# Performance work log

Hardware: AMD Instinct MI355X
Metric: run time of the kernel (lower is better)

The kernel has to match this reference:

```python
import jax, jax.numpy as jnp
import numpy as np

F_, H_, W_ = 8, 24, 24          # video_shape
KS, DIL = 3, 1                  # kernel_size, dilation (cubic)
HEADS, DH, DIM = 8, 64, 512
N_TOK = F_ * H_ * W_            # 4608 video tokens (+1 BOS)
PAD = DIL * (KS - 1) // 2
SCALE = DH ** -0.5


def _geometry():
    """Precompute im2col gather indices into the padded volume and the causal mask."""
    fp, hp, wp = F_ + 2 * PAD, H_ + 2 * PAD, W_ + 2 * PAD
    tg, ig, jg = np.meshgrid(np.arange(F_), np.arange(H_), np.arange(W_), indexing='ij')
    a = np.arange(KS) * DIL
    at, ai, aj = np.meshgrid(a, a, a, indexing='ij')  # window offsets
    # query (t,i,j) in original coords == window start in padded coords
    tc = tg.reshape(-1, 1) + at.reshape(1, -1)  # [N, K3]
    ic = ig.reshape(-1, 1) + ai.reshape(1, -1)
    jc = jg.reshape(-1, 1) + aj.reshape(1, -1)
    idx = (tc * hp + ic) * wp + jc              # flat index into padded volume
    # token-id volume padded with sentinel N_TOK (matches F.pad value=max_num_tokens)
    tok = np.full((fp, hp, wp), N_TOK, dtype=np.int64)
    tok[PAD:PAD + F_, PAD:PAD + H_, PAD:PAD + W_] = np.arange(N_TOK).reshape(F_, H_, W_)
    unfolded = tok.reshape(-1)[idx]             # [N, K3]
    causal = np.arange(N_TOK)[:, None] < unfolded  # True = masked (padding is N_TOK > all)
    mask = np.concatenate([np.zeros((N_TOK, 1), bool), causal], axis=1)  # BOS never masked
    return idx, mask

_IDX_NP, _MASK_NP = _geometry()


def setup_inputs() -> dict:
    key = jax.random.key(0)
    ks = jax.random.split(key, 6)
    n = N_TOK + 1
    return {
        'x': jax.random.normal(ks[0], (1, n, DIM), jnp.float32),
        'w_q': jax.random.normal(ks[1], (DIM, HEADS * DH), jnp.float32) * 0.02,
        'w_kv': jax.random.normal(ks[2], (DIM, 2 * HEADS * DH), jnp.float32) * 0.02,
        'w_talk': jax.random.normal(ks[3], (HEADS, HEADS), jnp.float32) * 0.1,
        'w_out': jax.random.normal(ks[4], (HEADS * DH, DIM), jnp.float32) * 0.02,
        'b_out': jnp.zeros((DIM,), jnp.float32),
    }


def reference(x, w_q, w_kv, w_talk, w_out, b_out):
    idx = jnp.asarray(_IDX_NP)
    mask = jnp.asarray(_MASK_NP)
    b, n, _ = x.shape
    bh = b * HEADS
    fp, hp, wp = F_ + 2 * PAD, H_ + 2 * PAD, W_ + 2 * PAD

    q = x @ w_q                                  # [b, n, h*d]
    k, v = jnp.split(x @ w_kv, 2, axis=-1)

    def to_heads(t):
        return t.reshape(b, n, HEADS, DH).transpose(0, 2, 1, 3).reshape(bh, n, DH)

    q, k, v = map(to_heads, (q, k, v))
    q = q[:, 1:] * SCALE                         # drop BOS query
    k_bos, v_bos = k[:, :1], v[:, :1]            # [bh, 1, d]
    k, v = k[:, 1:], v[:, 1:]

    def pad_unfold(t):
        vol = t.reshape(bh, F_, H_, W_, DH)
        vol = jnp.pad(vol, ((0, 0), (PAD, PAD), (PAD, PAD), (PAD, PAD), (0, 0)))
        flat = vol.reshape(bh, fp * hp * wp, DH)
        return flat[:, idx]                      # [bh, N, K3, d]

    k_unf, v_unf = pad_unfold(k), pad_unfold(v)
    k_full = jnp.concatenate([jnp.broadcast_to(k_bos[:, None], (bh, N_TOK, 1, DH)), k_unf], axis=2)
    v_full = jnp.concatenate([jnp.broadcast_to(v_bos[:, None], (bh, N_TOK, 1, DH)), v_unf], axis=2)

    sim = jnp.einsum('bid,bijd->bij', q, k_full)           # [bh, N, 1+K3]
    sim = jnp.where(mask[None], -jnp.finfo(sim.dtype).max, sim)
    attn = jax.nn.softmax(sim, axis=-1)
    attn = attn.reshape(b, HEADS, N_TOK, -1)
    attn = jnp.einsum('gh,bhij->bgij', w_talk, attn)       # talking heads (1x1 conv)
    attn = attn.reshape(bh, N_TOK, -1)

    out = jnp.einsum('bij,bijd->bid', attn, v_full)        # [bh, N, d]
    out = jnp.concatenate([v_bos, out], axis=1)            # BOS output = v_bos
    out = out.reshape(b, HEADS, n, DH).transpose(0, 2, 1, 3).reshape(b, n, HEADS * DH)
    return out @ w_out + b_out
```

## Files before the change

### kernel.cpp

```cpp
#include <hip/hip_runtime.h>
#include <cfloat>
#include <cmath>

#define F_   8
#define H_   24
#define W_   24
#define NTOK 4608
#define NSEQ 4609
#define MPAD 4736
#define DIM  512
#define QKVC 1536
#define NNB  28
#define SCALEF 0.125f

typedef unsigned short ushort_t;
typedef __attribute__((ext_vector_type(8))) short short8v;
typedef __attribute__((ext_vector_type(8))) unsigned short ushort8v;
typedef __attribute__((ext_vector_type(4))) float floatx4;

typedef const __attribute__((address_space(1))) unsigned int guint_t;
typedef __attribute__((address_space(3))) unsigned int luint_t;

__device__ __forceinline__ float bf2f(unsigned short u) {
    return __uint_as_float(((unsigned)u) << 16);
}
__device__ __forceinline__ unsigned short f2bf(float f) {
    unsigned u = __float_as_uint(f);
    unsigned r = (u + 0x7FFFu + ((u >> 16) & 1u)) >> 16;
    return (unsigned short)r;
}

#define XBLK 1184
#define CONV_BLOCKS (XBLK + 192 + 64)

__global__ __launch_bounds__(256) void conv_k(
    const float* __restrict__ x, const float* __restrict__ wq,
    const float* __restrict__ wkv, const float* __restrict__ wout,
    ushort_t* __restrict__ xb, ushort_t* __restrict__ wcatT,
    ushort_t* __restrict__ woutT)
{
    const int bid = blockIdx.x, tid = threadIdx.x;
    __shared__ ushort_t tile[64][72];

    if (bid < XBLK) {
        int e0 = (bid * 256 + tid) * 8;
        int row = e0 >> 9;
        float4 a = make_float4(0.f, 0.f, 0.f, 0.f);
        float4 b = make_float4(0.f, 0.f, 0.f, 0.f);
        if (row < NSEQ) {
            a = *reinterpret_cast<const float4*>(&x[e0]);
            b = *reinterpret_cast<const float4*>(&x[e0 + 4]);
        }
        ushort8v o;
        o[0] = f2bf(a.x); o[1] = f2bf(a.y); o[2] = f2bf(a.z); o[3] = f2bf(a.w);
        o[4] = f2bf(b.x); o[5] = f2bf(b.y); o[6] = f2bf(b.z); o[7] = f2bf(b.w);
        *reinterpret_cast<ushort8v*>(&xb[e0]) = o;
        return;
    }

    int blk2 = bid - XBLK;
    const float* src; int ld, cb; ushort_t* dst; int k0;
    if (blk2 < 192) {
        int nt = blk2 >> 3, kt = blk2 & 7;
        int n0 = nt * 64;
        if (n0 < 512) { src = wq;  ld = 512;  cb = n0; }
        else          { src = wkv; ld = 1024; cb = n0 - 512; }
        dst = wcatT + (size_t)n0 * 512;
        k0 = kt * 64;
    } else {
        int b3 = blk2 - 192;
        int nt = b3 >> 3, kt = b3 & 7;
        src = wout; ld = 512; cb = nt * 64;
        dst = woutT + (size_t)(nt * 64) * 512;
        k0 = kt * 64;
    }

    {
        int r = tid >> 4, c4 = (tid & 15) * 4;
        #pragma unroll
        for (int p = 0; p < 4; ++p) {
            int rr = r + p * 16;
            float4 v = *reinterpret_cast<const float4*>(&src[(size_t)(k0 + rr) * ld + cb + c4]);
            tile[c4 + 0][rr] = f2bf(v.x);
            tile[c4 + 1][rr] = f2bf(v.y);
            tile[c4 + 2][rr] = f2bf(v.z);
            tile[c4 + 3][rr] = f2bf(v.w);
        }
    }
    __syncthreads();
    {
        int nl = tid >> 3, ks = (tid & 7) * 8;
        #pragma unroll
        for (int rep = 0; rep < 2; ++rep) {
            int nn = nl + rep * 32;
            ushort8v vv = *reinterpret_cast<const ushort8v*>(&tile[nn][ks]);
            *reinterpret_cast<ushort8v*>(&dst[(size_t)nn * 512 + k0 + ks]) = vv;
        }
    }
}

template<int BM, bool F32OUT>
__global__ __launch_bounds__(256, 4) void gemm_k(
    const ushort_t* __restrict__ A,
    const ushort_t* __restrict__ BT,
    const float* __restrict__ bias,
    void* __restrict__ Cv, int ldc)
{
    __shared__ ushort_t sA[BM * 64];
    __shared__ ushort_t sB[128 * 64];
    const int tid = threadIdx.x;

    const int nwg = gridDim.x * gridDim.y;
    const int orig = blockIdx.y * gridDim.x + blockIdx.x;
    const int xcd = orig & 7;
    const int qq = nwg >> 3, rr8 = nwg & 7;
    const int wg = (xcd < rr8 ? xcd * (qq + 1) : rr8 * (qq + 1) + (xcd - rr8) * qq)
                   + (orig >> 3);
    const int row0 = (wg / gridDim.x) * BM;
    const int col0 = (wg % gridDim.x) * 128;

    const int wid = tid >> 6, lane = tid & 63;
    const int wr = wid >> 1, wc = wid & 1;
    const int l15 = lane & 15, kp = lane >> 4;
    constexpr int MR = BM / 32;

    floatx4 acc[MR][4];
    #pragma unroll
    for (int m = 0; m < MR; ++m)
        #pragma unroll
        for (int n = 0; n < 4; ++n)
            acc[m][n] = (floatx4){0.f, 0.f, 0.f, 0.f};

    const ushort_t* Abase = A + (size_t)row0 * 512;
    const ushort_t* Bbase = BT + (size_t)col0 * 512;

    for (int kt = 0; kt < 8; ++kt) {
        const int k0 = kt * 64;
        #pragma unroll
        for (int rnd = 0; rnd < BM / 32; ++rnd) {
            int r = rnd * 32 + (tid >> 3);
            int gs = (tid & 7) ^ (r & 7);
            __builtin_amdgcn_global_load_lds(
                (guint_t*)(Abase + (size_t)r * 512 + k0 + gs * 8),
                (luint_t*)(sA + r * 64 + (tid & 7) * 8), 16, 0, 0);
        }
        #pragma unroll
        for (int rnd = 0; rnd < 4; ++rnd) {
            int r = rnd * 32 + (tid >> 3);
            int gs = (tid & 7) ^ (r & 7);
            __builtin_amdgcn_global_load_lds(
                (guint_t*)(Bbase + (size_t)r * 512 + k0 + gs * 8),
                (luint_t*)(sB + r * 64 + (tid & 7) * 8), 16, 0, 0);
        }
        __syncthreads();

        #pragma unroll
        for (int kk = 0; kk < 2; ++kk) {
            short8v af[MR], bfr[4];
            #pragma unroll
            for (int m = 0; m < MR; ++m) {
                int r = wr * (BM / 2) + m * 16 + l15;
                int slot = kk * 4 + kp;
                af[m] = *(const short8v*)&sA[r * 64 + ((slot ^ (r & 7)) << 3)];
            }
            #pragma unroll
            for (int n = 0; n < 4; ++n) {
                int r = wc * 64 + n * 16 + l15;
                int slot = kk * 4 + kp;
                bfr[n] = *(const short8v*)&sB[r * 64 + ((slot ^ (r & 7)) << 3)];
            }
            #pragma unroll
            for (int m = 0; m < MR; ++m)
                #pragma unroll
                for (int n = 0; n < 4; ++n)
                    acc[m][n] = __builtin_amdgcn_mfma_f32_16x16x32_bf16(
                        af[m], bfr[n], acc[m][n], 0, 0, 0);
        }
        __syncthreads();
    }

    if (!F32OUT) {
        ushort_t* C = (ushort_t*)Cv;
        #pragma unroll
        for (int m = 0; m < MR; ++m) {
            int rb = row0 + wr * (BM / 2) + m * 16 + kp * 4;
            #pragma unroll
            for (int n = 0; n < 4; ++n) {
                int col = col0 + wc * 64 + n * 16 + l15;
                #pragma unroll
                for (int q = 0; q < 4; ++q)
                    C[(size_t)(rb + q) * ldc + col] = f2bf(acc[m][n][q]);
            }
        }
    } else {
        float* C = (float*)Cv;
        #pragma unroll
        for (int m = 0; m < MR; ++m) {
            int rb = row0 + wr * (BM / 2) + m * 16 + kp * 4;
            #pragma unroll
            for (int n = 0; n < 4; ++n) {
                int col = col0 + wc * 64 + n * 16 + l15;
                float bv = bias[col];
                #pragma unroll
                for (int q = 0; q < 4; ++q)
                    if (rb + q < NSEQ)
                        C[(size_t)(rb + q) * ldc + col] = acc[m][n][q] + bv;
            }
        }
    }
}

__global__ __launch_bounds__(256) void attn_k(
    const ushort_t* __restrict__ qkv,
    const float* __restrict__ wtalk,
    ushort_t* __restrict__ outh)
{
    const int lane = threadIdx.x & 63;
    const int bid0 = blockIdx.x;
    const int bswz = (bid0 & 7) * (gridDim.x >> 3) + (bid0 >> 3);
    const int i = bswz * 4 + (threadIdx.x >> 6);
    const int h = lane >> 3, s = lane & 7;

    const int t = i / (H_ * W_), rem = i % (H_ * W_);
    const int yy = rem / W_, xx = rem % W_;

    int rowj = -1;
    if (lane == 0) rowj = 0;
    else if (lane < NNB) {
        int e = lane - 1;
        int dt = e / 9 - 1, dy = (e / 3) % 3 - 1, dx = e % 3 - 1;
        int nt = t + dt, ny = yy + dy, nx = xx + dx;
        bool valid = ((unsigned)nt < (unsigned)F_) && ((unsigned)ny < (unsigned)H_) &&
                     ((unsigned)nx < (unsigned)W_);
        int u = (nt * H_ + ny) * W_ + nx;
        rowj = (valid && u <= i) ? (u + 1) : -1;
    }

    int rows[NNB];
    #pragma unroll
    for (int j = 0; j < NNB; ++j) rows[j] = __shfl(rowj, j, 64);

    float qf[8];
    {
        ushort8v qv = *(const ushort8v*)&qkv[(size_t)(i + 1) * QKVC + lane * 8];
        #pragma unroll
        for (int e = 0; e < 8; ++e) qf[e] = bf2f(qv[e]);
    }

    float ps[NNB];
    #pragma unroll
    for (int j = 0; j < NNB; ++j) {
        int r = rows[j] < 0 ? 0 : rows[j];
        ushort8v kv = *(const ushort8v*)&qkv[(size_t)r * QKVC + 512 + lane * 8];
        float a = 0.f;
        #pragma unroll
        for (int e = 0; e < 8; ++e) a += qf[e] * bf2f(kv[e]);
        ps[j] = a;
    }

    float v1[14];
    {
        bool hi = (s & 1) != 0;
        #pragma unroll
        for (int m = 0; m < 14; ++m) {
            float keep = hi ? ps[2 * m + 1] : ps[2 * m];
            float oth  = hi ? ps[2 * m]     : ps[2 * m + 1];
            v1[m] = keep + __shfl_xor(oth, 1, 64);
        }
    }
    float v2[8];
    {
        bool hi = (s & 2) != 0;
        #pragma unroll
        for (int m = 0; m < 7; ++m) {
            float keep = hi ? v1[2 * m + 1] : v1[2 * m];
            float oth  = hi ? v1[2 * m]     : v1[2 * m + 1];
            v2[m] = keep + __shfl_xor(oth, 2, 64);
        }
        v2[7] = 0.f;
    }
    float simk[4];
    {
        bool hi = (s & 4) != 0;
        #pragma unroll
        for (int k = 0; k < 4; ++k) {
            float keep = hi ? v2[2 * k + 1] : v2[2 * k];
            float oth  = hi ? v2[2 * k]     : v2[2 * k + 1];
            simk[k] = keep + __shfl_xor(oth, 4, 64);
        }
    }
    #pragma unroll
    for (int k = 0; k < 4; ++k) {
        int j = s + 8 * k;
        int rj = __shfl(rowj, j, 64);
        simk[k] = (rj >= 0) ? simk[k] * SCALEF : -FLT_MAX;
    }

    float mx = fmaxf(fmaxf(simk[0], simk[1]), fmaxf(simk[2], simk[3]));
    mx = fmaxf(mx, __shfl_xor(mx, 1, 64));
    mx = fmaxf(mx, __shfl_xor(mx, 2, 64));
    mx = fmaxf(mx, __shfl_xor(mx, 4, 64));
    float att[4];
    float S = 0.f;
    #pragma unroll
    for (int k = 0; k < 4; ++k) { att[k] = __expf(simk[k] - mx); S += att[k]; }
    S += __shfl_xor(S, 1, 64);
    S += __shfl_xor(S, 2, 64);
    S += __shfl_xor(S, 4, 64);
    float inv = 1.f / S;
    #pragma unroll
    for (int k = 0; k < 4; ++k) att[k] *= inv;

    float wtg[8];
    #pragma unroll
    for (int hh = 0; hh < 8; ++hh) wtg[hh] = wtalk[h * 8 + hh];
    float pk[4];
    #pragma unroll
    for (int k = 0; k < 4; ++k) {
        float acc = 0.f;
        #pragma unroll
        for (int hh = 0; hh < 8; ++hh)
            acc += wtg[hh] * __shfl(att[k], hh * 8 + s, 64);
        pk[k] = acc;
    }

    float o[8];
    #pragma unroll
    for (int e = 0; e < 8; ++e) o[e] = 0.f;
    #pragma unroll
    for (int j = 0; j < NNB; ++j) {
        float pj = __shfl(pk[j >> 3], h * 8 + (j & 7), 64);
        int r = rows[j] < 0 ? 0 : rows[j];
        ushort8v vv = *(const ushort8v*)&qkv[(size_t)r * QKVC + 1024 + lane * 8];
        #pragma unroll
        for (int e = 0; e < 8; ++e) o[e] += pj * bf2f(vv[e]);
    }

    ushort8v ov;
    #pragma unroll
    for (int e = 0; e < 8; ++e) ov[e] = f2bf(o[e]);
    *(ushort8v*)&outh[(size_t)(i + 1) * DIM + lane * 8] = ov;

    if (i == 0) {
        ushort8v bv = *(const ushort8v*)&qkv[1024 + lane * 8];
        *(ushort8v*)&outh[lane * 8] = bv;
    }
}

extern "C" void kernel_launch(void* const* d_in, const int* in_sizes, int n_in,
                              void* d_out, int out_size, void* d_ws, size_t ws_size,
                              hipStream_t stream) {
    const float* x     = (const float*)d_in[0];
    const float* wq    = (const float*)d_in[1];
    const float* wkv   = (const float*)d_in[2];
    const float* wtalk = (const float*)d_in[3];
    const float* wout  = (const float*)d_in[4];
    const float* bout  = (const float*)d_in[5];
    float* out = (float*)d_out;

    ushort_t* xb    = (ushort_t*)d_ws;
    ushort_t* wcatT = xb    + (size_t)MPAD * 512;
    ushort_t* woutT = wcatT + (size_t)QKVC * 512;
    ushort_t* qkv   = woutT + (size_t)512 * 512;
    ushort_t* outh  = qkv   + (size_t)MPAD * QKVC;

    dim3 blk(256);
    conv_k<<<CONV_BLOCKS, blk, 0, stream>>>(x, wq, wkv, wout, xb, wcatT, woutT);
    gemm_k<64, false><<<dim3(12, 74), blk, 0, stream>>>(xb, wcatT, nullptr, qkv, QKVC);
    attn_k<<<dim3(NTOK / 4), blk, 0, stream>>>(qkv, wtalk, outh);
    gemm_k<64, true><<<dim3(4, 74), blk, 0, stream>>>(outh, woutT, bout, out, DIM);
}
```

Baseline: 53.30 us.

## Fuse fp32-to-bf16 conversion of x into QKV GEMM A-tile staging

Removes the separate x conversion pass from the conversion kernel. The QKV GEMM now loads fp32 rows of x directly, packs them to bf16 by truncation with a byte permute, and writes them into swizzled LDS, which drops one full write and reread of the activations. The attention kernel also skips K/V loads for masked neighbours and hoists the probability shuffles out of the V loop. The trade-off is that the GEMM A-tile now goes through registers instead of async global-to-LDS loads, reads twice the bytes per tile, and rounds by truncation rather than round-to-nearest.

```diff
diff --git a/kernel.cpp b/kernel.cpp
--- a/kernel.cpp
+++ b/kernel.cpp
@@ -29,36 +29,20 @@
     unsigned r = (u + 0x7FFFu + ((u >> 16) & 1u)) >> 16;
     return (unsigned short)r;
 }
-
-#define XBLK 1184
-#define CONV_BLOCKS (XBLK + 192 + 64)
+__device__ __forceinline__ unsigned pk2(float a, float b) {
+    return __builtin_amdgcn_perm(__float_as_uint(b), __float_as_uint(a), 0x07060302u);
+}
+
+#define CONV_BLOCKS 256
 
 __global__ __launch_bounds__(256) void conv_k(
-    const float* __restrict__ x, const float* __restrict__ wq,
-    const float* __restrict__ wkv, const float* __restrict__ wout,
-    ushort_t* __restrict__ xb, ushort_t* __restrict__ wcatT,
-    ushort_t* __restrict__ woutT)
+    const float* __restrict__ wq, const float* __restrict__ wkv,
+    const float* __restrict__ wout,
+    ushort_t* __restrict__ wcatT, ushort_t* __restrict__ woutT)
 {
-    const int bid = blockIdx.x, tid = threadIdx.x;
+    const int blk2 = blockIdx.x, tid = threadIdx.x;
     __shared__ ushort_t tile[64][72];
 
-    if (bid < XBLK) {
-        int e0 = (bid * 256 + tid) * 8;
-        int row = e0 >> 9;
-        float4 a = make_float4(0.f, 0.f, 0.f, 0.f);
-        float4 b = make_float4(0.f, 0.f, 0.f, 0.f);
-        if (row < NSEQ) {
-            a = *reinterpret_cast<const float4*>(&x[e0]);
-            b = *reinterpret_cast<const float4*>(&x[e0 + 4]);
-        }
-        ushort8v o;
-        o[0] = f2bf(a.x); o[1] = f2bf(a.y); o[2] = f2bf(a.z); o[3] = f2bf(a.w);
-        o[4] = f2bf(b.x); o[5] = f2bf(b.y); o[6] = f2bf(b.z); o[7] = f2bf(b.w);
-        *reinterpret_cast<ushort8v*>(&xb[e0]) = o;
-        return;
-    }
-
-    int blk2 = bid - XBLK;
     const float* src; int ld, cb; ushort_t* dst; int k0;
     if (blk2 < 192) {
         int nt = blk2 >> 3, kt = blk2 & 7;
@@ -99,9 +83,9 @@
     }
 }
 
-template<int BM, bool F32OUT>
+template<int BM, bool F32A, bool F32OUT>
 __global__ __launch_bounds__(256, 4) void gemm_k(
-    const ushort_t* __restrict__ A,
+    const void* __restrict__ Av,
     const ushort_t* __restrict__ BT,
     const float* __restrict__ bias,
     void* __restrict__ Cv, int ldc)
@@ -131,19 +115,12 @@
         for (int n = 0; n < 4; ++n)
             acc[m][n] = (floatx4){0.f, 0.f, 0.f, 0.f};
 
-    const ushort_t* Abase = A + (size_t)row0 * 512;
+    const ushort_t* Ab = (const ushort_t*)Av;
+    const float*    Af = (const float*)Av;
     const ushort_t* Bbase = BT + (size_t)col0 * 512;
 
     for (int kt = 0; kt < 8; ++kt) {
         const int k0 = kt * 64;
-        #pragma unroll
-        for (int rnd = 0; rnd < BM / 32; ++rnd) {
-            int r = rnd * 32 + (tid >> 3);
-            int gs = (tid & 7) ^ (r & 7);
-            __builtin_amdgcn_global_load_lds(
-                (guint_t*)(Abase + (size_t)r * 512 + k0 + gs * 8),
-                (luint_t*)(sA + r * 64 + (tid & 7) * 8), 16, 0, 0);
-        }
         #pragma unroll
         for (int rnd = 0; rnd < 4; ++rnd) {
             int r = rnd * 32 + (tid >> 3);
@@ -151,6 +128,36 @@
             __builtin_amdgcn_global_load_lds(
                 (guint_t*)(Bbase + (size_t)r * 512 + k0 + gs * 8),
                 (luint_t*)(sB + r * 64 + (tid & 7) * 8), 16, 0, 0);
+        }
+        if constexpr (F32A) {
+            static_assert(BM == 64, "F32A staging assumes BM==64");
+            int r = tid >> 2;
+            int kq = (tid & 3) << 4;
+            float4 f0 = make_float4(0.f,0.f,0.f,0.f), f1 = f0, f2 = f0, f3 = f0;
+            if (row0 + r < NSEQ) {
+                const float* sp = Af + (size_t)(row0 + r) * 512 + k0 + kq;
+                f0 = *(const float4*)(sp + 0);
+                f1 = *(const float4*)(sp + 4);
+                f2 = *(const float4*)(sp + 8);
+                f3 = *(const float4*)(sp + 12);
+            }
+            uint4 lo, hi;
+            lo.x = pk2(f0.x, f0.y); lo.y = pk2(f0.z, f0.w);
+            lo.z = pk2(f1.x, f1.y); lo.w = pk2(f1.z, f1.w);
+            hi.x = pk2(f2.x, f2.y); hi.y = pk2(f2.z, f2.w);
+            hi.z = pk2(f3.x, f3.y); hi.w = pk2(f3.z, f3.w);
+            int slot0 = kq >> 3;
+            *(uint4*)&sA[r * 64 + ((slot0       ^ (r & 7)) << 3)] = lo;
+            *(uint4*)&sA[r * 64 + (((slot0 | 1) ^ (r & 7)) << 3)] = hi;
+        } else {
+            #pragma unroll
+            for (int rnd = 0; rnd < BM / 32; ++rnd) {
+                int r = rnd * 32 + (tid >> 3);
+                int gs = (tid & 7) ^ (r & 7);
+                __builtin_amdgcn_global_load_lds(
+                    (guint_t*)(Ab + (size_t)(row0 + r) * 512 + k0 + gs * 8),
+                    (luint_t*)(sA + r * 64 + (tid & 7) * 8), 16, 0, 0);
+            }
         }
         __syncthreads();
 
@@ -250,11 +257,12 @@
     float ps[NNB];
     #pragma unroll
     for (int j = 0; j < NNB; ++j) {
-        int r = rows[j] < 0 ? 0 : rows[j];
-        ushort8v kv = *(const ushort8v*)&qkv[(size_t)r * QKVC + 512 + lane * 8];
         float a = 0.f;
-        #pragma unroll
-        for (int e = 0; e < 8; ++e) a += qf[e] * bf2f(kv[e]);
+        if (rows[j] >= 0) {
+            ushort8v kv = *(const ushort8v*)&qkv[(size_t)rows[j] * QKVC + 512 + lane * 8];
+            #pragma unroll
+            for (int e = 0; e < 8; ++e) a += qf[e] * bf2f(kv[e]);
+        }
         ps[j] = a;
     }
 
@@ -324,16 +332,21 @@
         pk[k] = acc;
     }
 
+    float pj[NNB];
+    #pragma unroll
+    for (int j = 0; j < NNB; ++j)
+        pj[j] = __shfl(pk[j >> 3], h * 8 + (j & 7), 64);
+
     float o[8];
     #pragma unroll
     for (int e = 0; e < 8; ++e) o[e] = 0.f;
     #pragma unroll
     for (int j = 0; j < NNB; ++j) {
-        float pj = __shfl(pk[j >> 3], h * 8 + (j & 7), 64);
-        int r = rows[j] < 0 ? 0 : rows[j];
-        ushort8v vv = *(const ushort8v*)&qkv[(size_t)r * QKVC + 1024 + lane * 8];
-        #pragma unroll
-        for (int e = 0; e < 8; ++e) o[e] += pj * bf2f(vv[e]);
+        if (rows[j] >= 0) {
+            ushort8v vv = *(const ushort8v*)&qkv[(size_t)rows[j] * QKVC + 1024 + lane * 8];
+            #pragma unroll
+            for (int e = 0; e < 8; ++e) o[e] += pj[j] * bf2f(vv[e]);
+        }
     }
 
     ushort8v ov;
@@ -358,15 +371,14 @@
     const float* bout  = (const float*)d_in[5];
     float* out = (float*)d_out;
 
-    ushort_t* xb    = (ushort_t*)d_ws;
-    ushort_t* wcatT = xb    + (size_t)MPAD * 512;
+    ushort_t* wcatT = (ushort_t*)d_ws;
     ushort_t* woutT = wcatT + (size_t)QKVC * 512;
     ushort_t* qkv   = woutT + (size_t)512 * 512;
     ushort_t* outh  = qkv   + (size_t)MPAD * QKVC;
 
     dim3 blk(256);
-    conv_k<<<CONV_BLOCKS, blk, 0, stream>>>(x, wq, wkv, wout, xb, wcatT, woutT);
-    gemm_k<64, false><<<dim3(12, 74), blk, 0, stream>>>(xb, wcatT, nullptr, qkv, QKVC);
+    conv_k<<<CONV_BLOCKS, blk, 0, stream>>>(wq, wkv, wout, wcatT, woutT);
+    gemm_k<64, true, false><<<dim3(12, 74), blk, 0, stream>>>(x, wcatT, nullptr, qkv, QKVC);
     attn_k<<<dim3(NTOK / 4), blk, 0, stream>>>(qkv, wtalk, outh);
-    gemm_k<64, true><<<dim3(4, 74), blk, 0, stream>>>(outh, woutT, bout, out, DIM);
-}
+    gemm_k<64, false, true><<<dim3(4, 74), blk, 0, stream>>>(outh, woutT, bout, out, DIM);
+}
```

New measurement: 55.15 us. 3.5% more time.

## Process two adjacent queries per wavefront sharing a 3x3x4 neighbor union

Applied to the files above, without the earlier changes.

Each wavefront now handles two horizontally adjacent query tokens. It loads the union of their neighborhoods once, 37 rows (BOS plus 3x3x4), instead of 2x28 separate K and V row loads. Each loaded K and V row is reused for both queries' dot products and output accumulations. The grid is halved. This cuts global and L2 gather traffic and address work, at the cost of more registers per thread, which may lower occupancy. It also leaves fewer blocks to hide latency.

```diff
diff --git a/kernel.cpp b/kernel.cpp
--- a/kernel.cpp
+++ b/kernel.cpp
@@ -11,6 +11,7 @@
 #define DIM  512
 #define QKVC 1536
 #define NNB  28
+#define NU   37
 #define SCALEF 0.125f
 
 typedef unsigned short ushort_t;
@@ -218,130 +219,196 @@
     const int lane = threadIdx.x & 63;
     const int bid0 = blockIdx.x;
     const int bswz = (bid0 & 7) * (gridDim.x >> 3) + (bid0 >> 3);
-    const int i = bswz * 4 + (threadIdx.x >> 6);
+    const int wj = bswz * 4 + (threadIdx.x >> 6);
+    const int iA = wj * 2, iB = iA + 1;
     const int h = lane >> 3, s = lane & 7;
 
-    const int t = i / (H_ * W_), rem = i % (H_ * W_);
-    const int yy = rem / W_, xx = rem % W_;
-
-    int rowj = -1;
-    if (lane == 0) rowj = 0;
+    const int t = iA / (H_ * W_), rem = iA % (H_ * W_);
+    const int yy = rem / W_, xA = rem % W_;
+
+    int rowu_ln = 0;
+    if (lane >= 1 && lane < NU) {
+        int e = lane - 1;
+        int dt = e / 12 - 1, dy = (e % 12) / 4 - 1, dx = (e & 3) - 1;
+        int nt = t + dt, ny = yy + dy, nx = xA + dx;
+        bool valid = ((unsigned)nt < (unsigned)F_) && ((unsigned)ny < (unsigned)H_) &&
+                     ((unsigned)nx < (unsigned)W_);
+        rowu_ln = valid ? ((nt * H_ + ny) * W_ + nx + 1) : 0;
+    }
+    int rowjA_ln = -1, rowjB_ln = -1;
+    if (lane == 0) { rowjA_ln = 0; rowjB_ln = 0; }
     else if (lane < NNB) {
         int e = lane - 1;
         int dt = e / 9 - 1, dy = (e / 3) % 3 - 1, dx = e % 3 - 1;
-        int nt = t + dt, ny = yy + dy, nx = xx + dx;
-        bool valid = ((unsigned)nt < (unsigned)F_) && ((unsigned)ny < (unsigned)H_) &&
-                     ((unsigned)nx < (unsigned)W_);
-        int u = (nt * H_ + ny) * W_ + nx;
-        rowj = (valid && u <= i) ? (u + 1) : -1;
-    }
-
-    int rows[NNB];
-    #pragma unroll
-    for (int j = 0; j < NNB; ++j) rows[j] = __shfl(rowj, j, 64);
-
-    float qf[8];
+        {
+            int nt = t + dt, ny = yy + dy, nx = xA + dx;
+            bool valid = ((unsigned)nt < (unsigned)F_) && ((unsigned)ny < (unsigned)H_) &&
+                         ((unsigned)nx < (unsigned)W_);
+            int u = (nt * H_ + ny) * W_ + nx;
+            rowjA_ln = (valid && u <= iA) ? (u + 1) : -1;
+        }
+        {
+            int nt = t + dt, ny = yy + dy, nx = xA + 1 + dx;
+            bool valid = ((unsigned)nt < (unsigned)F_) && ((unsigned)ny < (unsigned)H_) &&
+                         ((unsigned)nx < (unsigned)W_);
+            int u = (nt * H_ + ny) * W_ + nx;
+            rowjB_ln = (valid && u <= iB) ? (u + 1) : -1;
+        }
+    }
+
+    float qfA[8], qfB[8];
     {
-        ushort8v qv = *(const ushort8v*)&qkv[(size_t)(i + 1) * QKVC + lane * 8];
-        #pragma unroll
-        for (int e = 0; e < 8; ++e) qf[e] = bf2f(qv[e]);
-    }
-
-    float ps[NNB];
-    #pragma unroll
-    for (int j = 0; j < NNB; ++j) {
-        int r = rows[j] < 0 ? 0 : rows[j];
+        ushort8v qa = *(const ushort8v*)&qkv[(size_t)(iA + 1) * QKVC + lane * 8];
+        ushort8v qb = *(const ushort8v*)&qkv[(size_t)(iB + 1) * QKVC + lane * 8];
+        #pragma unroll
+        for (int e = 0; e < 8; ++e) { qfA[e] = bf2f(qa[e]); qfB[e] = bf2f(qb[e]); }
+    }
+
+    float psA[NNB], psB[NNB];
+    #pragma unroll
+    for (int j = 0; j < NNB; ++j) { psA[j] = 0.f; psB[j] = 0.f; }
+    #pragma unroll
+    for (int u = 0; u < NU; ++u) {
+        int r = __shfl(rowu_ln, u, 64);
         ushort8v kv = *(const ushort8v*)&qkv[(size_t)r * QKVC + 512 + lane * 8];
-        float a = 0.f;
-        #pragma unroll
-        for (int e = 0; e < 8; ++e) a += qf[e] * bf2f(kv[e]);
-        ps[j] = a;
-    }
-
-    float v1[14];
-    {
-        bool hi = (s & 1) != 0;
-        #pragma unroll
-        for (int m = 0; m < 14; ++m) {
-            float keep = hi ? ps[2 * m + 1] : ps[2 * m];
-            float oth  = hi ? ps[2 * m]     : ps[2 * m + 1];
-            v1[m] = keep + __shfl_xor(oth, 1, 64);
-        }
-    }
-    float v2[8];
-    {
-        bool hi = (s & 2) != 0;
-        #pragma unroll
-        for (int m = 0; m < 7; ++m) {
-            float keep = hi ? v1[2 * m + 1] : v1[2 * m];
-            float oth  = hi ? v1[2 * m]     : v1[2 * m + 1];
-            v2[m] = keep + __shfl_xor(oth, 2, 64);
-        }
-        v2[7] = 0.f;
-    }
-    float simk[4];
-    {
-        bool hi = (s & 4) != 0;
+        float kf[8];
+        #pragma unroll
+        for (int e = 0; e < 8; ++e) kf[e] = bf2f(kv[e]);
+        if (u == 0) {
+            float a = 0.f, b = 0.f;
+            #pragma unroll
+            for (int e = 0; e < 8; ++e) { a += qfA[e] * kf[e]; b += qfB[e] * kf[e]; }
+            psA[0] = a; psB[0] = b;
+        } else {
+            const int e = u - 1;
+            const int dtp = e / 12, dyp = (e % 12) / 4, dxq = e & 3;
+            if (dxq <= 2) {
+                const int jA = 1 + dtp * 9 + dyp * 3 + dxq;
+                float a = 0.f;
+                #pragma unroll
+                for (int ee = 0; ee < 8; ++ee) a += qfA[ee] * kf[ee];
+                psA[jA] = a;
+            }
+            if (dxq >= 1) {
+                const int jB = 1 + dtp * 9 + dyp * 3 + (dxq - 1);
+                float b = 0.f;
+                #pragma unroll
+                for (int ee = 0; ee < 8; ++ee) b += qfB[ee] * kf[ee];
+                psB[jB] = b;
+            }
+        }
+    }
+
+    float wtg[8];
+    #pragma unroll
+    for (int hh = 0; hh < 8; ++hh) wtg[hh] = wtalk[h * 8 + hh];
+
+    auto finish = [&](float* ps, int rowj_ln, float* pk) {
+        float v1[14];
+        {
+            bool hi = (s & 1) != 0;
+            #pragma unroll
+            for (int m = 0; m < 14; ++m) {
+                float keep = hi ? ps[2 * m + 1] : ps[2 * m];
+                float oth  = hi ? ps[2 * m]     : ps[2 * m + 1];
+                v1[m] = keep + __shfl_xor(oth, 1, 64);
+            }
+        }
+        float v2[8];
+        {
+            bool hi = (s & 2) != 0;
+            #pragma unroll
+            for (int m = 0; m < 7; ++m) {
+                float keep = hi ? v1[2 * m + 1] : v1[2 * m];
+                float oth  = hi ? v1[2 * m]     : v1[2 * m + 1];
+                v2[m] = keep + __shfl_xor(oth, 2, 64);
+            }
+            v2[7] = 0.f;
+        }
+        float simk[4];
+        {
+            bool hi = (s & 4) != 0;
+            #pragma unroll
+            for (int k = 0; k < 4; ++k) {
+                float keep = hi ? v2[2 * k + 1] : v2[2 * k];
+                float oth  = hi ? v2[2 * k]     : v2[2 * k + 1];
+                simk[k] = keep + __shfl_xor(oth, 4, 64);
+            }
+        }
         #pragma unroll
         for (int k = 0; k < 4; ++k) {
-            float keep = hi ? v2[2 * k + 1] : v2[2 * k];
-            float oth  = hi ? v2[2 * k]     : v2[2 * k + 1];
-            simk[k] = keep + __shfl_xor(oth, 4, 64);
-        }
-    }
-    #pragma unroll
-    for (int k = 0; k < 4; ++k) {
-        int j = s + 8 * k;
-        int rj = __shfl(rowj, j, 64);
-        simk[k] = (rj >= 0) ? simk[k] * SCALEF : -FLT_MAX;
-    }
-
-    float mx = fmaxf(fmaxf(simk[0], simk[1]), fmaxf(simk[2], simk[3]));
-    mx = fmaxf(mx, __shfl_xor(mx, 1, 64));
-    mx = fmaxf(mx, __shfl_xor(mx, 2, 64));
-    mx = fmaxf(mx, __shfl_xor(mx, 4, 64));
-    float att[4];
-    float S = 0.f;
-    #pragma unroll
-    for (int k = 0; k < 4; ++k) { att[k] = __expf(simk[k] - mx); S += att[k]; }
-    S += __shfl_xor(S, 1, 64);
-    S += __shfl_xor(S, 2, 64);
-    S += __shfl_xor(S, 4, 64);
-    float inv = 1.f / S;
-    #pragma unroll
-    for (int k = 0; k < 4; ++k) att[k] *= inv;
-
-    float wtg[8];
-    #pragma unroll
-    for (int hh = 0; hh < 8; ++hh) wtg[hh] = wtalk[h * 8 + hh];
-    float pk[4];
-    #pragma unroll
-    for (int k = 0; k < 4; ++k) {
-        float acc = 0.f;
-        #pragma unroll
-        for (int hh = 0; hh < 8; ++hh)
-            acc += wtg[hh] * __shfl(att[k], hh * 8 + s, 64);
-        pk[k] = acc;
-    }
-
-    float o[8];
-    #pragma unroll
-    for (int e = 0; e < 8; ++e) o[e] = 0.f;
-    #pragma unroll
-    for (int j = 0; j < NNB; ++j) {
-        float pj = __shfl(pk[j >> 3], h * 8 + (j & 7), 64);
-        int r = rows[j] < 0 ? 0 : rows[j];
+            int j = s + 8 * k;
+            int rj = __shfl(rowj_ln, j, 64);
+            simk[k] = (rj >= 0) ? simk[k] * SCALEF : -FLT_MAX;
+        }
+        float mx = fmaxf(fmaxf(simk[0], simk[1]), fmaxf(simk[2], simk[3]));
+        mx = fmaxf(mx, __shfl_xor(mx, 1, 64));
+        mx = fmaxf(mx, __shfl_xor(mx, 2, 64));
+        mx = fmaxf(mx, __shfl_xor(mx, 4, 64));
+        float att[4];
+        float S = 0.f;
+        #pragma unroll
+        for (int k = 0; k < 4; ++k) { att[k] = __expf(simk[k] - mx); S += att[k]; }
+        S += __shfl_xor(S, 1, 64);
+        S += __shfl_xor(S, 2, 64);
+        S += __shfl_xor(S, 4, 64);
+        float inv = 1.f / S;
+        #pragma unroll
+        for (int k = 0; k < 4; ++k) att[k] *= inv;
+        #pragma unroll
+        for (int k = 0; k < 4; ++k) {
+            float acc = 0.f;
+            #pragma unroll
+            for (int hh = 0; hh < 8; ++hh)
+                acc += wtg[hh] * __shfl(att[k], hh * 8 + s, 64);
+            pk[k] = acc;
+        }
+    };
+
+    float pkA[4], pkB[4];
+    finish(psA, rowjA_ln, pkA);
+    finish(psB, rowjB_ln, pkB);
+
+    float oA[8], oB[8];
+    #pragma unroll
+    for (int e = 0; e < 8; ++e) { oA[e] = 0.f; oB[e] = 0.f; }
+    #pragma unroll
+    for (int u = 0; u < NU; ++u) {
+        int r = __shfl(rowu_ln, u, 64);
         ushort8v vv = *(const ushort8v*)&qkv[(size_t)r * QKVC + 1024 + lane * 8];
-        #pragma unroll
-        for (int e = 0; e < 8; ++e) o[e] += pj * bf2f(vv[e]);
-    }
-
-    ushort8v ov;
-    #pragma unroll
-    for (int e = 0; e < 8; ++e) ov[e] = f2bf(o[e]);
-    *(ushort8v*)&outh[(size_t)(i + 1) * DIM + lane * 8] = ov;
-
-    if (i == 0) {
+        float vf[8];
+        #pragma unroll
+        for (int e = 0; e < 8; ++e) vf[e] = bf2f(vv[e]);
+        if (u == 0) {
+            float pa = __shfl(pkA[0], h * 8, 64);
+            float pb = __shfl(pkB[0], h * 8, 64);
+            #pragma unroll
+            for (int e = 0; e < 8; ++e) { oA[e] += pa * vf[e]; oB[e] += pb * vf[e]; }
+        } else {
+            const int e = u - 1;
+            const int dtp = e / 12, dyp = (e % 12) / 4, dxq = e & 3;
+            if (dxq <= 2) {
+                const int jA = 1 + dtp * 9 + dyp * 3 + dxq;
+                float pa = __shfl(pkA[jA >> 3], h * 8 + (jA & 7), 64);
+                #pragma unroll
+                for (int ee = 0; ee < 8; ++ee) oA[ee] += pa * vf[ee];
+            }
+            if (dxq >= 1) {
+                const int jB = 1 + dtp * 9 + dyp * 3 + (dxq - 1);
+                float pb = __shfl(pkB[jB >> 3], h * 8 + (jB & 7), 64);
+                #pragma unroll
+                for (int ee = 0; ee < 8; ++ee) oB[ee] += pb * vf[ee];
+            }
+        }
+    }
+
+    ushort8v ovA, ovB;
+    #pragma unroll
+    for (int e = 0; e < 8; ++e) { ovA[e] = f2bf(oA[e]); ovB[e] = f2bf(oB[e]); }
+    *(ushort8v*)&outh[(size_t)(iA + 1) * DIM + lane * 8] = ovA;
+    *(ushort8v*)&outh[(size_t)(iB + 1) * DIM + lane * 8] = ovB;
+
+    if (iA == 0) {
         ushort8v bv = *(const ushort8v*)&qkv[1024 + lane * 8];
         *(ushort8v*)&outh[lane * 8] = bv;
     }
@@ -367,6 +434,6 @@
     dim3 blk(256);
     conv_k<<<CONV_BLOCKS, blk, 0, stream>>>(x, wq, wkv, wout, xb, wcatT, woutT);
     gemm_k<64, false><<<dim3(12, 74), blk, 0, stream>>>(xb, wcatT, nullptr, qkv, QKVC);
-    attn_k<<<dim3(NTOK / 4), blk, 0, stream>>>(qkv, wtalk, outh);
+    attn_k<<<dim3(NTOK / 8), blk, 0, stream>>>(qkv, wtalk, outh);
     gemm_k<64, true><<<dim3(4, 74), blk, 0, stream>>>(outh, woutT, bout, out, DIM);
 }
```

Result: slower. 67.46 us (+26.6%).
